# Kernel tuning notes

Hardware: AMD Instinct MI355X
Metric: run time of the kernel (lower is better)

Reference implementation:

```python
import jax, jax.numpy as jnp
import numpy as np

N_NODES = 100000
N_EDGES = 640000
N_GRAPHS = 2048
HID = 128
L = 3


def setup_inputs() -> dict:
    key = jax.random.key(0)
    ks = jax.random.split(key, 24)
    f32 = jnp.float32
    x = jax.random.normal(ks[0], (N_NODES, 7), dtype=f32)
    edge_attr = jax.random.normal(ks[1], (N_EDGES, 3), dtype=f32)
    edge_index = jax.random.randint(ks[2], (2, N_EDGES), 0, N_NODES, dtype=jnp.int32)
    batch = jnp.sort(jax.random.randint(ks[3], (N_NODES,), 0, N_GRAPHS, dtype=jnp.int32))

    def lin(k, fi, fo):
        return jax.random.normal(k, (fi, fo), dtype=f32) / jnp.sqrt(jnp.asarray(fi, f32))

    inp = dict(x=x, edge_attr=edge_attr, edge_index=edge_index, batch=batch)
    inp["node_w"] = lin(ks[4], 7, HID); inp["node_b"] = jnp.zeros((HID,), f32)
    inp["ew1"] = lin(ks[5], 3, HID);   inp["eb1"] = jnp.zeros((HID,), f32)
    inp["ew2"] = lin(ks[6], HID, HID); inp["eb2"] = jnp.zeros((HID,), f32)
    inp["cw1"] = jnp.stack([lin(ks[7 + i], HID, HID) for i in range(L)])
    inp["cb1"] = jnp.zeros((L, HID), f32)
    inp["cw2"] = jnp.stack([lin(ks[10 + i], HID, HID) for i in range(L)])
    inp["cb2"] = jnp.zeros((L, HID), f32)
    inp["clw1"] = lin(ks[13], HID, 64); inp["clb1"] = jnp.zeros((64,), f32)
    inp["clw2"] = lin(ks[14], 64, 1);   inp["clb2"] = jnp.zeros((1,), f32)
    inp["rw1"] = lin(ks[15], HID, 64);  inp["rb1"] = jnp.zeros((64,), f32)
    inp["rw2"] = lin(ks[16], 64, 1);    inp["rb2"] = jnp.zeros((1,), f32)
    return inp


def reference(x, edge_attr, node_w, node_b, ew1, eb1, ew2, eb2,
              cw1, cb1, cw2, cb2, clw1, clb1, clw2, clb2,
              rw1, rb1, rw2, rb2, edge_index, batch):
    relu = jax.nn.relu
    # encoders
    h = x @ node_w + node_b                                   # [N, H]
    e = relu(edge_attr @ ew1 + eb1) @ ew2 + eb2               # [E, H]
    src, dst = edge_index[0], edge_index[1]
    for l in range(L):
        # GINEConv (eps=0): out = MLP(h_i + sum_j ReLU(h_j + e_ji))
        m = relu(h[src] + e)                                  # [E, H] gather + edge add
        agg = jax.ops.segment_sum(m, dst, num_segments=N_NODES)
        z = h + agg
        h = relu(z @ cw1[l] + cb1[l]) @ cw2[l] + cb2[l]
        h = relu(h)                                           # dropout = identity (eval)
    # global mean pool
    ones = jnp.ones((h.shape[0],), h.dtype)
    counts = jax.ops.segment_sum(ones, batch, num_segments=N_GRAPHS)
    g = jax.ops.segment_sum(h, batch, num_segments=N_GRAPHS) / jnp.maximum(counts, 1.0)[:, None]
    success_logit = (relu(g @ clw1 + clb1) @ clw2 + clb2)[:, 0]
    route_length = (relu(g @ rw1 + rb1) @ rw2 + rb2)[:, 0]
    return success_logit, route_length
```

## Files before the change

kernel.cpp:

```cpp
#include <hip/hip_runtime.h>

#define HID 128
#define LDP 136

typedef short s16x8 __attribute__((ext_vector_type(8)));
typedef float f32x4 __attribute__((ext_vector_type(4)));

__device__ __forceinline__ float bf2f(unsigned int u) {
  union { unsigned int i; float f; } v; v.i = u << 16; return v.f;
}
__device__ __forceinline__ float asf(unsigned int u) {
  union { unsigned int i; float f; } v; v.i = u; return v.f;
}
__device__ __forceinline__ unsigned short f2bf(float f) {
  union { float f; unsigned int i; } v; v.f = f;
  unsigned int r = v.i + 0x7fffu + ((v.i >> 16) & 1u);
  return (unsigned short)(r >> 16);
}

__global__ void k_zero4(float4* __restrict__ p, size_t n4) {
  size_t i = (size_t)blockIdx.x * blockDim.x + threadIdx.x;
  if (i < n4) p[i] = (float4){0.f, 0.f, 0.f, 0.f};
}

__global__ void k_hist(const int* __restrict__ dst, int* __restrict__ deg, int nE) {
  int e = blockIdx.x * blockDim.x + threadIdx.x;
  if (e < nE) atomicAdd(&deg[dst[e]], 1);
}

__global__ void k_scanA(const int* __restrict__ deg, int* __restrict__ bsum) {
  __shared__ int ss[256];
  int t = threadIdx.x;
  ss[t] = deg[blockIdx.x * 256 + t];
  __syncthreads();
  for (int off = 128; off; off >>= 1) {
    if (t < off) ss[t] += ss[t + off];
    __syncthreads();
  }
  if (t == 0) bsum[blockIdx.x] = ss[0];
}

__global__ void k_scanB(const int* __restrict__ bsum, int* __restrict__ bsumx, int NB) {
  __shared__ int sd[512];
  int t = threadIdx.x;
  int v = (t < NB) ? bsum[t] : 0;
  sd[t] = v;
  __syncthreads();
  for (int off = 1; off < 512; off <<= 1) {
    int a = (t >= off) ? sd[t - off] : 0;
    __syncthreads();
    sd[t] += a;
    __syncthreads();
  }
  if (t < NB) bsumx[t] = sd[t] - v;
}

__global__ void k_scanC(const int* __restrict__ deg, const int* __restrict__ bsumx,
                        int* __restrict__ cursor, int* __restrict__ rowptr) {
  __shared__ int ss[256];
  int t = threadIdx.x, i = blockIdx.x * 256 + t;
  int v = deg[i];
  ss[t] = v;
  __syncthreads();
  for (int off = 1; off < 256; off <<= 1) {
    int a = (t >= off) ? ss[t - off] : 0;
    __syncthreads();
    ss[t] += a;
    __syncthreads();
  }
  int ex = ss[t] - v + bsumx[blockIdx.x];
  cursor[i] = ex;
  rowptr[i] = ex;
}

__global__ void k_scatter(const int* __restrict__ src, const int* __restrict__ dst,
                          const float* __restrict__ ea, int* __restrict__ cursor,
                          int* __restrict__ src_s, float* __restrict__ ea_s, int nE) {
  int e = blockIdx.x * blockDim.x + threadIdx.x;
  if (e >= nE) return;
  int d = dst[e];
  int pos = atomicAdd(&cursor[d], 1);
  src_s[pos] = src[e];
  ea_s[(size_t)pos * 3 + 0] = ea[(size_t)e * 3 + 0];
  ea_s[(size_t)pos * 3 + 1] = ea[(size_t)e * 3 + 1];
  ea_s[(size_t)pos * 3 + 2] = ea[(size_t)e * 3 + 2];
}

__global__ void k_prep_w(const float* __restrict__ ew2, const float* __restrict__ cw1,
                         const float* __restrict__ cw2, unsigned short* __restrict__ wT) {
  int idx = blockIdx.x * blockDim.x + threadIdx.x;
  if (idx >= 7 * 16384) return;
  int m = idx >> 14, i = idx & 16383;
  int n = i >> 7, k = i & 127;
  const float* s = (m == 0) ? ew2 : (m <= 3 ? cw1 + (size_t)(m - 1) * 16384
                                            : cw2 + (size_t)(m - 4) * 16384);
  wT[idx] = f2bf(s[k * 128 + n]);
}

__global__ void k_node_enc(const float* __restrict__ x, const float* __restrict__ w,
                           const float* __restrict__ b, unsigned short* __restrict__ h16, int nN) {
  int idx = blockIdx.x * blockDim.x + threadIdx.x;
  if (idx >= nN * HID) return;
  int i = idx >> 7, j = idx & 127;
  float acc = b[j];
  const float* xr = x + (size_t)i * 7;
#pragma unroll
  for (int k = 0; k < 7; ++k) acc += xr[k] * w[k * HID + j];
  h16[idx] = f2bf(acc);
}

__global__ void __launch_bounds__(256) k_edge_gemm(
    const float* __restrict__ ea_s, const float* __restrict__ ew1, const float* __restrict__ eb1,
    const unsigned short* __restrict__ w2t, const float* __restrict__ eb2,
    unsigned short* __restrict__ e16, int nE) {
  __shared__ __attribute__((aligned(16))) unsigned short ts1[128 * LDP];
  __shared__ float eaL[384];
  int tid = threadIdx.x;
  int e0 = blockIdx.x * 128;
  for (int i = tid; i < 384; i += 256) eaL[i] = ea_s[(size_t)e0 * 3 + i];
  __syncthreads();
  {
    int j = tid & 127, r0 = (tid >> 7) * 64;
    float wa = ew1[j], wb = ew1[HID + j], wc = ew1[2 * HID + j], bj = eb1[j];
    for (int r = r0; r < r0 + 64; ++r) {
      float a = bj + eaL[r * 3] * wa + eaL[r * 3 + 1] * wb + eaL[r * 3 + 2] * wc;
      ts1[r * LDP + j] = f2bf(fmaxf(a, 0.f));
    }
  }
  __syncthreads();
  int wave = tid >> 6, lane = tid & 63;
  int l15 = lane & 15, quad = lane >> 4;
  int rbase = (wave >> 1) * 64, nbase = (wave & 1) * 64;
  f32x4 acc[4][4];
#pragma unroll
  for (int i = 0; i < 4; ++i)
#pragma unroll
    for (int j = 0; j < 4; ++j) acc[i][j] = (f32x4){0.f, 0.f, 0.f, 0.f};
  for (int kc = 0; kc < 4; ++kc) {
    int k0 = kc * 32 + quad * 8;
    s16x8 af[4], bf[4];
#pragma unroll
    for (int t = 0; t < 4; ++t)
      af[t] = *(const s16x8*)&ts1[(rbase + t * 16 + l15) * LDP + k0];
#pragma unroll
    for (int t = 0; t < 4; ++t)
      bf[t] = *(const s16x8*)&w2t[(size_t)(nbase + t * 16 + l15) * HID + k0];
#pragma unroll
    for (int i = 0; i < 4; ++i)
#pragma unroll
      for (int j = 0; j < 4; ++j)
        acc[i][j] = __builtin_amdgcn_mfma_f32_16x16x32_bf16(af[i], bf[j], acc[i][j], 0, 0, 0);
  }
  float ebv[4];
#pragma unroll
  for (int t = 0; t < 4; ++t) ebv[t] = eb2[nbase + t * 16 + l15];
#pragma unroll
  for (int tr = 0; tr < 4; ++tr)
#pragma unroll
    for (int reg = 0; reg < 4; ++reg) {
      int row = rbase + tr * 16 + quad * 4 + reg;
#pragma unroll
      for (int tc = 0; tc < 4; ++tc) {
        int col = nbase + tc * 16 + l15;
        e16[(size_t)(e0 + row) * HID + col] = f2bf(acc[tr][tc][reg] + ebv[tc]);
      }
    }
}

__global__ void __launch_bounds__(256) k_conv_csr(
    const unsigned short* __restrict__ h16in, const unsigned short* __restrict__ e16,
    const int* __restrict__ src_s, const int* __restrict__ rowptr,
    const unsigned short* __restrict__ w1t, const float* __restrict__ b1,
    const unsigned short* __restrict__ w2t, const float* __restrict__ b2,
    unsigned short* __restrict__ h16out, int nN) {
  __shared__ __attribute__((aligned(16))) unsigned short zs[32 * LDP];
  __shared__ int rpS[4][12];
  int tid = threadIdx.x;
  int n0 = blockIdx.x * 32;
  int wave = tid >> 6, lane = tid & 63;
  {
    int c2 = lane * 2;
    int wbase = wave * 8;
    int nodeBase = n0 + wbase;
    int nCnt = nN - nodeBase; if (nCnt > 8) nCnt = 8; if (nCnt < 0) nCnt = 0;
#pragma unroll
    for (int i = 0; i < 8; ++i) {
      int n = nodeBase + i;
      unsigned int hv = 0u;
      if (n < nN) hv = *(const unsigned int*)&h16in[(size_t)n * HID + c2];
      *(unsigned int*)&zs[(wbase + i) * LDP + c2] = hv;
    }
    if (lane < 9) {
      int i = (lane < nCnt) ? lane : nCnt;
      rpS[wave][lane] = (nCnt > 0) ? rowptr[nodeBase + i] : 0;
    }
    int eBeg = rpS[wave][0];
    int eEnd = rpS[wave][8];
    if (nCnt > 0 && eBeg < eEnd) {
      float a0 = 0.f, a1 = 0.f;
      int ni = 0;
      int rpEnd = rpS[wave][1];
      int sv0[8], sv1[8];
      unsigned int ev0[8], hv0[8], ev1[8], hv1[8];

#define LOAD_S(svv, base)                                            \
  _Pragma("unroll")                                                  \
  for (int i = 0; i < 8; ++i) {                                      \
    int ix = (base) + i; if (ix >= eEnd) ix = eEnd - 1;              \
    svv[i] = src_s[ix];                                              \
  }
#define LOAD_EH(evv, hvv, svv, base)                                 \
  _Pragma("unroll")                                                  \
  for (int i = 0; i < 8; ++i) {                                      \
    int ix = (base) + i; if (ix >= eEnd) ix = eEnd - 1;              \
    evv[i] = *(const unsigned int*)&e16[(size_t)ix * HID + c2];      \
    hvv[i] = *(const unsigned int*)&h16in[(size_t)svv[i] * HID + c2];\
  }
#define FLUSH()                                                      \
  { int row = wbase + ni;                                            \
    unsigned int z = *(const unsigned int*)&zs[row * LDP + c2];      \
    float z0 = asf(z << 16) + a0, z1 = asf(z & 0xffff0000u) + a1;    \
    *(unsigned int*)&zs[row * LDP + c2] =                            \
        (unsigned int)f2bf(z0) | ((unsigned int)f2bf(z1) << 16);     \
    a0 = 0.f; a1 = 0.f; }
#define FOLD(evv, hvv, base)                                         \
  { int cnt = eEnd - (base); if (cnt > 8) cnt = 8;                   \
    _Pragma("unroll")                                                \
    for (int i = 0; i < 8; ++i) if (i < cnt) {                       \
      int eg = (base) + i;                                           \
      while (eg >= rpEnd) { FLUSH(); ++ni; rpEnd = rpS[wave][ni + 1]; } \
      a0 += fmaxf(asf(hvv[i] << 16) + asf(evv[i] << 16), 0.f);       \
      a1 += fmaxf(asf(hvv[i] & 0xffff0000u) + asf(evv[i] & 0xffff0000u), 0.f); \
    } }

      LOAD_S(sv0, eBeg)
      LOAD_S(sv1, eBeg + 8)
      LOAD_EH(ev0, hv0, sv0, eBeg)
      for (int e = eBeg; e < eEnd; e += 16) {
        if (e + 16 < eEnd) LOAD_S(sv0, e + 16)
        if (e + 8 < eEnd)  LOAD_EH(ev1, hv1, sv1, e + 8)
        FOLD(ev0, hv0, e)
        if (e + 8 < eEnd) {
          if (e + 24 < eEnd) LOAD_S(sv1, e + 24)
          if (e + 16 < eEnd) LOAD_EH(ev0, hv0, sv0, e + 16)
          FOLD(ev1, hv1, e + 8)
        }
      }
      FLUSH()
#undef LOAD_S
#undef LOAD_EH
#undef FLUSH
#undef FOLD
    }
  }
  __syncthreads();
  int l15 = lane & 15, quad = lane >> 4;
  int rbase = (wave >> 1) * 16, nbase = (wave & 1) * 64;
  f32x4 acc[4];
#pragma unroll
  for (int j = 0; j < 4; ++j) acc[j] = (f32x4){0.f, 0.f, 0.f, 0.f};
  for (int kc = 0; kc < 4; ++kc) {
    int k0 = kc * 32 + quad * 8;
    s16x8 af, bf[4];
    af = *(const s16x8*)&zs[(rbase + l15) * LDP + k0];
#pragma unroll
    for (int t = 0; t < 4; ++t)
      bf[t] = *(const s16x8*)&w1t[(size_t)(nbase + t * 16 + l15) * HID + k0];
#pragma unroll
    for (int j = 0; j < 4; ++j)
      acc[j] = __builtin_amdgcn_mfma_f32_16x16x32_bf16(af, bf[j], acc[j], 0, 0, 0);
  }
  __syncthreads();
  {
    float bv[4];
#pragma unroll
    for (int t = 0; t < 4; ++t) bv[t] = b1[nbase + t * 16 + l15];
#pragma unroll
    for (int tc = 0; tc < 4; ++tc)
#pragma unroll
      for (int reg = 0; reg < 4; ++reg) {
        int row = rbase + quad * 4 + reg;
        int col = nbase + tc * 16 + l15;
        zs[row * LDP + col] = f2bf(fmaxf(acc[tc][reg] + bv[tc], 0.f));
      }
  }
  __syncthreads();
#pragma unroll
  for (int j = 0; j < 4; ++j) acc[j] = (f32x4){0.f, 0.f, 0.f, 0.f};
  for (int kc = 0; kc < 4; ++kc) {
    int k0 = kc * 32 + quad * 8;
    s16x8 af, bf[4];
    af = *(const s16x8*)&zs[(rbase + l15) * LDP + k0];
#pragma unroll
    for (int t = 0; t < 4; ++t)
      bf[t] = *(const s16x8*)&w2t[(size_t)(nbase + t * 16 + l15) * HID + k0];
#pragma unroll
    for (int j = 0; j < 4; ++j)
      acc[j] = __builtin_amdgcn_mfma_f32_16x16x32_bf16(af, bf[j], acc[j], 0, 0, 0);
  }
  {
    float bv[4];
#pragma unroll
    for (int t = 0; t < 4; ++t) bv[t] = b2[nbase + t * 16 + l15];
#pragma unroll
    for (int reg = 0; reg < 4; ++reg) {
      int grow = n0 + rbase + quad * 4 + reg;
      if (grow < nN) {
#pragma unroll
        for (int tc = 0; tc < 4; ++tc) {
          int col = nbase + tc * 16 + l15;
          h16out[(size_t)grow * HID + col] = f2bf(fmaxf(acc[tc][reg] + bv[tc], 0.f));
        }
      }
    }
  }
}

__global__ void k_counts(const int* __restrict__ batch, int* __restrict__ cnts, int nN) {
  int i = blockIdx.x * blockDim.x + threadIdx.x;
  if (i < nN) atomicAdd(&cnts[batch[i]], 1);
}

__global__ void __launch_bounds__(256) k_pool2(
    const unsigned short* __restrict__ h16, const int* __restrict__ batch,
    float* __restrict__ g, int nN) {
  __shared__ int bL[128];
  int tid = threadIdx.x;
  int n0 = blockIdx.x * 128;
  if (tid < 128) {
    int n = n0 + tid;
    bL[tid] = (n < nN) ? batch[n] : -1;
  }
  __syncthreads();
  int half = tid >> 7, col = tid & 127;
  int rs = half * 64;
  int cur = -1;
  float s = 0.f;
  for (int r = rs; r < rs + 64; ++r) {
    int b = bL[r];
    float v = (b >= 0) ? bf2f((unsigned int)h16[(size_t)(n0 + r) * HID + col]) : 0.f;
    if (b != cur) {
      if (cur >= 0) atomicAdd(&g[(size_t)cur * HID + col], s);
      cur = b; s = v;
    } else s += v;
  }
  if (cur >= 0) atomicAdd(&g[(size_t)cur * HID + col], s);
}

__global__ void __launch_bounds__(128) k_head(
    const float* __restrict__ g, const int* __restrict__ counts,
    const float* __restrict__ clw1, const float* __restrict__ clb1,
    const float* __restrict__ clw2, const float* __restrict__ clb2,
    const float* __restrict__ rw1, const float* __restrict__ rb1,
    const float* __restrict__ rw2, const float* __restrict__ rb2,
    float* __restrict__ out, int nG) {
  __shared__ float gs[HID];
  int b = blockIdx.x;
  int tid = threadIdx.x;
  float cnt = fmaxf((float)counts[b], 1.f);
  gs[tid] = g[b * HID + tid] / cnt;
  __syncthreads();
  int wave = tid >> 6, lane = tid & 63;
  const float* w1 = wave ? rw1 : clw1;
  const float* b1 = wave ? rb1 : clb1;
  const float* w2 = wave ? rw2 : clw2;
  const float* b2 = wave ? rb2 : clb2;
  float acc = b1[lane];
  for (int k = 0; k < HID; ++k) acc += gs[k] * w1[k * 64 + lane];
  acc = fmaxf(acc, 0.f) * w2[lane];
#pragma unroll
  for (int off = 32; off; off >>= 1) acc += __shfl_down(acc, off);
  if (lane == 0) out[wave * nG + b] = acc + b2[0];
}

extern "C" void kernel_launch(void* const* d_in, const int* in_sizes, int n_in,
                              void* d_out, int out_size, void* d_ws, size_t ws_size,
                              hipStream_t stream) {
  const float* x      = (const float*)d_in[0];
  const float* ea     = (const float*)d_in[1];
  const int*   eidx   = (const int*)d_in[2];
  const int*   batch  = (const int*)d_in[3];
  const float* node_w = (const float*)d_in[4];
  const float* node_b = (const float*)d_in[5];
  const float* ew1    = (const float*)d_in[6];
  const float* eb1    = (const float*)d_in[7];
  const float* ew2    = (const float*)d_in[8];
  const float* eb2    = (const float*)d_in[9];
  const float* cw1    = (const float*)d_in[10];
  const float* cb1    = (const float*)d_in[11];
  const float* cw2    = (const float*)d_in[12];
  const float* cb2    = (const float*)d_in[13];
  const float* clw1   = (const float*)d_in[14];
  const float* clb1   = (const float*)d_in[15];
  const float* clw2   = (const float*)d_in[16];
  const float* clb2   = (const float*)d_in[17];
  const float* rw1    = (const float*)d_in[18];
  const float* rb1    = (const float*)d_in[19];
  const float* rw2    = (const float*)d_in[20];
  const float* rb2    = (const float*)d_in[21];
  float* out = (float*)d_out;

  int nN = in_sizes[3];
  int nE = in_sizes[2] / 2;
  int nG = out_size / 2;
  const int* src = eidx;
  const int* dst = eidx + nE;

  int NB = (nN + 255) / 256;
  int bins = NB * 256;

  size_t hN = (size_t)nN * HID;
  size_t gN = (size_t)nG * HID;
  float* g    = (float*)d_ws;
  int*   cnts = (int*)(g + gN);
  unsigned short* wT   = (unsigned short*)(cnts + nG);
  unsigned short* h16a = wT + 7 * 16384;
  unsigned short* h16b = h16a + hN;
  int* deg    = (int*)(h16b + hN);
  int* cursor = deg + bins;
  int* rowptr = cursor + bins;
  int* bsum   = rowptr + bins;
  int* bsumx  = bsum + 512;
  int* src_s  = bsumx + 512;
  float* ea_s = (float*)(src_s + nE);
  unsigned short* e16 = (unsigned short*)(ea_s + (size_t)3 * nE);

  k_zero4<<<(int)((bins / 4 + 255) / 256), 256, 0, stream>>>((float4*)deg, bins / 4);
  k_hist<<<(nE + 255) / 256, 256, 0, stream>>>(dst, deg, nE);
  k_scanA<<<NB, 256, 0, stream>>>(deg, bsum);
  k_scanB<<<1, 512, 0, stream>>>(bsum, bsumx, NB);
  k_scanC<<<NB, 256, 0, stream>>>(deg, bsumx, cursor, rowptr);
  k_scatter<<<(nE + 255) / 256, 256, 0, stream>>>(src, dst, ea, cursor, src_s, ea_s, nE);

  k_prep_w<<<(7 * 16384 + 255) / 256, 256, 0, stream>>>(ew2, cw1, cw2, wT);
  k_edge_gemm<<<nE / 128, 256, 0, stream>>>(ea_s, ew1, eb1, wT, eb2, e16, nE);
  k_node_enc<<<(nN * HID + 255) / 256, 256, 0, stream>>>(x, node_w, node_b, h16a, nN);

  unsigned short* hin  = h16a;
  unsigned short* hout = h16b;
  for (int l = 0; l < 3; ++l) {
    k_conv_csr<<<(nN + 31) / 32, 256, 0, stream>>>(
        hin, e16, src_s, rowptr,
        wT + (size_t)(1 + l) * 16384, cb1 + (size_t)l * HID,
        wT + (size_t)(4 + l) * 16384, cb2 + (size_t)l * HID, hout, nN);
    unsigned short* t = hin; hin = hout; hout = t;
  }

  k_zero4<<<(int)(((gN + nG) / 4 + 255) / 256), 256, 0, stream>>>((float4*)g, (gN + nG) / 4);
  k_counts<<<(nN + 255) / 256, 256, 0, stream>>>(batch, cnts, nN);
  k_pool2<<<(nN + 127) / 128, 256, 0, stream>>>(hin, batch, g, nN);
  k_head<<<nG, 128, 0, stream>>>(g, cnts, clw1, clb1, clw2, clb2,
                                 rw1, rb1, rw2, rb2, out, nG);
}
```

Measured before the change: 654.9 us.

## Restructure CSR edge aggregation to 16-byte loads with 4 edges per wave step

The per-wave edge aggregation in the conv kernel now splits each wave into four quads of 16 lanes. Each quad handles one edge per step and each lane loads 8 bf16 channels with a uint4 load, replacing the layout where all 64 lanes took 2 channels of one edge with 32-bit loads. Partial sums are combined across quads with xor shuffles when a node's edges end, and a three-stage software pipeline (index, payload, fold) hides gather latency. This cuts the number of load instructions and makes wider transactions, at the cost of shuffle reductions and idle quads on low-degree nodes.

```diff
diff --git a/kernel.cpp b/kernel.cpp
--- a/kernel.cpp
+++ b/kernel.cpp
@@ -178,7 +178,9 @@
   int tid = threadIdx.x;
   int n0 = blockIdx.x * 32;
   int wave = tid >> 6, lane = tid & 63;
+  int l15 = lane & 15, quad = lane >> 4;
   {
+    int c16 = l15 * 8;
     int c2 = lane * 2;
     int wbase = wave * 8;
     int nodeBase = n0 + wbase;
@@ -194,67 +196,86 @@
       int i = (lane < nCnt) ? lane : nCnt;
       rpS[wave][lane] = (nCnt > 0) ? rowptr[nodeBase + i] : 0;
     }
-    int eBeg = rpS[wave][0];
-    int eEnd = rpS[wave][8];
-    if (nCnt > 0 && eBeg < eEnd) {
-      float a0 = 0.f, a1 = 0.f;
+    if (nCnt > 0) {
+      int gb = rpS[wave][0];
+      int gEnd = rpS[wave][8];
       int ni = 0;
-      int rpEnd = rpS[wave][1];
-      int sv0[8], sv1[8];
-      unsigned int ev0[8], hv0[8], ev1[8], hv1[8];
-
-#define LOAD_S(svv, base)                                            \
-  _Pragma("unroll")                                                  \
-  for (int i = 0; i < 8; ++i) {                                      \
-    int ix = (base) + i; if (ix >= eEnd) ix = eEnd - 1;              \
-    svv[i] = src_s[ix];                                              \
-  }
-#define LOAD_EH(evv, hvv, svv, base)                                 \
-  _Pragma("unroll")                                                  \
-  for (int i = 0; i < 8; ++i) {                                      \
-    int ix = (base) + i; if (ix >= eEnd) ix = eEnd - 1;              \
-    evv[i] = *(const unsigned int*)&e16[(size_t)ix * HID + c2];      \
-    hvv[i] = *(const unsigned int*)&h16in[(size_t)svv[i] * HID + c2];\
-  }
-#define FLUSH()                                                      \
-  { int row = wbase + ni;                                            \
-    unsigned int z = *(const unsigned int*)&zs[row * LDP + c2];      \
-    float z0 = asf(z << 16) + a0, z1 = asf(z & 0xffff0000u) + a1;    \
-    *(unsigned int*)&zs[row * LDP + c2] =                            \
-        (unsigned int)f2bf(z0) | ((unsigned int)f2bf(z1) << 16);     \
-    a0 = 0.f; a1 = 0.f; }
-#define FOLD(evv, hvv, base)                                         \
-  { int cnt = eEnd - (base); if (cnt > 8) cnt = 8;                   \
-    _Pragma("unroll")                                                \
-    for (int i = 0; i < 8; ++i) if (i < cnt) {                       \
-      int eg = (base) + i;                                           \
-      while (eg >= rpEnd) { FLUSH(); ++ni; rpEnd = rpS[wave][ni + 1]; } \
-      a0 += fmaxf(asf(hvv[i] << 16) + asf(evv[i] << 16), 0.f);       \
-      a1 += fmaxf(asf(hvv[i] & 0xffff0000u) + asf(evv[i] & 0xffff0000u), 0.f); \
+      while (ni < 8 && rpS[wave][ni + 1] <= gb) ++ni;
+      int re = (ni < 8) ? rpS[wave][ni + 1] : gb;
+      float acc[8];
+#pragma unroll
+      for (int j = 0; j < 8; ++j) acc[j] = 0.f;
+
+      int eixA = 0, eixB = 0, eixC = 0, svA = 0, svB = 0, svC = 0;
+      int niA = 0, niB = 0, niC = 0;
+      bool vA = false, vB = false, vC = false, lA = false, lB = false, lC = false;
+      uint4 evA, hvA, evB, hvB;
+      bool aA = false, aB = false, aC = false;
+
+#define PS(eix, sv, v, l, nis)                                   \
+  { int gq = gb + quad;                                          \
+    eix = (gq < re) ? gq : (re - 1);                             \
+    v = (gq < re);                                               \
+    l = (gb + 4 >= re);                                          \
+    nis = ni;                                                    \
+    sv = src_s[eix];                                             \
+    gb = (gb + 4 < re) ? (gb + 4) : re;                          \
+    if (gb >= re) {                                              \
+      while (ni < 8 && rpS[wave][ni + 1] <= gb) ++ni;            \
+      if (ni < 8) re = rpS[wave][ni + 1];                        \
     } }
-
-      LOAD_S(sv0, eBeg)
-      LOAD_S(sv1, eBeg + 8)
-      LOAD_EH(ev0, hv0, sv0, eBeg)
-      for (int e = eBeg; e < eEnd; e += 16) {
-        if (e + 16 < eEnd) LOAD_S(sv0, e + 16)
-        if (e + 8 < eEnd)  LOAD_EH(ev1, hv1, sv1, e + 8)
-        FOLD(ev0, hv0, e)
-        if (e + 8 < eEnd) {
-          if (e + 24 < eEnd) LOAD_S(sv1, e + 24)
-          if (e + 16 < eEnd) LOAD_EH(ev0, hv0, sv0, e + 16)
-          FOLD(ev1, hv1, e + 8)
-        }
+#define PEH(ev, hv, eix, sv)                                     \
+  { ev = *(const uint4*)&e16[(size_t)eix * HID + c16];           \
+    hv = *(const uint4*)&h16in[(size_t)sv * HID + c16]; }
+#define FOLDX(ev, hv, v, l, nis)                                 \
+  { const unsigned int* ew = (const unsigned int*)&ev;           \
+    const unsigned int* hw = (const unsigned int*)&hv;           \
+    if (v) {                                                     \
+      _Pragma("unroll")                                          \
+      for (int j = 0; j < 4; ++j) {                              \
+        acc[2*j]   += fmaxf(asf(hw[j] << 16) + asf(ew[j] << 16), 0.f); \
+        acc[2*j+1] += fmaxf(asf(hw[j] & 0xffff0000u) + asf(ew[j] & 0xffff0000u), 0.f); \
+      }                                                          \
+    }                                                            \
+    if (l) {                                                     \
+      _Pragma("unroll")                                          \
+      for (int j = 0; j < 8; ++j) {                              \
+        acc[j] += __shfl_xor(acc[j], 16);                        \
+        acc[j] += __shfl_xor(acc[j], 32);                        \
+      }                                                          \
+      if (quad == 0) {                                           \
+        int row = wbase + nis;                                   \
+        uint4 z = *(const uint4*)&zs[row * LDP + c16];           \
+        unsigned int* zw = (unsigned int*)&z;                    \
+        _Pragma("unroll")                                        \
+        for (int j = 0; j < 4; ++j) {                            \
+          float z0 = asf(zw[j] << 16) + acc[2*j];                \
+          float z1 = asf(zw[j] & 0xffff0000u) + acc[2*j+1];      \
+          zw[j] = (unsigned int)f2bf(z0) | ((unsigned int)f2bf(z1) << 16); \
+        }                                                        \
+        *(uint4*)&zs[row * LDP + c16] = z;                       \
+      }                                                          \
+      _Pragma("unroll")                                          \
+      for (int j = 0; j < 8; ++j) acc[j] = 0.f;                  \
+    } }
+
+      if (gb < gEnd) { PS(eixA, svA, vA, lA, niA) aA = true; }
+      if (gb < gEnd) { PS(eixB, svB, vB, lB, niB) aB = true; }
+      if (aA) PEH(evA, hvA, eixA, svA)
+      while (aA) {
+        aC = (gb < gEnd);
+        if (aC) PS(eixC, svC, vC, lC, niC)
+        if (aB) PEH(evB, hvB, eixB, svB)
+        FOLDX(evA, hvA, vA, lA, niA)
+        aA = aB; evA = evB; hvA = hvB; vA = vB; lA = lB; niA = niB; eixA = eixB; svA = svB;
+        aB = aC; eixB = eixC; svB = svC; vB = vC; lB = lC; niB = niC;
       }
-      FLUSH()
-#undef LOAD_S
-#undef LOAD_EH
-#undef FLUSH
-#undef FOLD
-    }
-  }
-  __syncthreads();
-  int l15 = lane & 15, quad = lane >> 4;
+#undef PS
+#undef PEH
+#undef FOLDX
+    }
+  }
+  __syncthreads();
   int rbase = (wave >> 1) * 16, nbase = (wave & 1) * 64;
   f32x4 acc[4];
 #pragma unroll
```

Result: faster. 631.0 us (-3.7%).
